# Kernel tuning notes

Measured on AMD Instinct MI355X. Metric: run time of the kernel, lower is better.

## Reference

```python
import jax, jax.numpy as jnp
import numpy as np

N_BLOCKS = 8
N_WIRES = 24
GAMMA, BETA, ALPHA = 0.1, 0.6, 0.15


def _apply_ry(state, w, theta):
    # RY(theta) = [[cos(t/2), -sin(t/2)], [sin(t/2), cos(t/2)]] on wire w.
    c = jnp.cos(theta * 0.5)
    s = jnp.sin(theta * 0.5)
    st = jnp.moveaxis(state, w, 0)  # (2, ...)
    new = jnp.stack([c * st[0] - s * st[1], s * st[0] + c * st[1]])
    return jnp.moveaxis(new, 0, w)


def _apply_cnot(state, ctrl, tgt):
    # Flip target bit where control bit == 1.
    st = jnp.moveaxis(state, (ctrl, tgt), (0, 1))  # (2, 2, ...)
    new = jnp.stack([st[0], st[1, ::-1]])
    return jnp.moveaxis(new, (0, 1), (ctrl, tgt))


def setup_inputs() -> dict:
    key = jax.random.key(0)
    angles = jax.random.normal(key, (N_BLOCKS, N_WIRES), dtype=jnp.float32)
    return {"angles": angles}


def reference(angles):
    n_blocks, n_wires = angles.shape  # static
    # Initial state |0...0>; RY and CNOT are real, so the state stays real.
    state = jnp.zeros((2,) * n_wires, dtype=angles.dtype).at[(0,) * n_wires].set(1.0)
    for k in range(n_blocks):
        for w in range(n_wires):
            state = _apply_ry(state, w, angles[k, w])
        for w in range(n_wires - 1):  # circular=False -> linear chain
            state = _apply_cnot(state, w, w + 1)
    probs = (state.reshape(-1) ** 2).reshape(2 ** n_wires, 1)  # |amp|^2
    easy_scale = 2.0 ** (n_wires - 1)
    x = (BETA * jnp.tanh(GAMMA * easy_scale * probs)) ** ALPHA
    return x - jnp.mean(x)
```

## Files before the change

### kernel.cpp

```cpp
#include <hip/hip_runtime.h>

#define NB 8
#define SSIZE (1u << 24)


__global__ void k_prep(const float* __restrict__ ang, double* __restrict__ dws) {
    int t = threadIdx.x;
    if (t == 0) dws[0] = 0.0;
    if (t < NB * 24) {
        double a = 0.5 * (double)ang[t];
        dws[8 + t]   = cos(a);
        dws[200 + t] = sin(a);
    }
}


__device__ __forceinline__ unsigned sw(unsigned f) {
    return f ^ (((f >> 3) ^ (f >> 5)) & 7u);
}

__device__ __forceinline__ void ry2d(double& a0, double& a1, double c, double s, bool ctl) {
    double w0 = c * a0 - s * a1;
    double w1 = s * a0 + c * a1;
    a0 = ctl ? w1 : w0;
    a1 = ctl ? w0 : w1;
}

template<int TB, int MODE>
__device__ __forceinline__ void stage8d(double4* x, double c, double s) {
#pragma unroll
    for (int j0 = 0; j0 < 8; ++j0) {
        if (j0 & (1 << TB)) continue;
        const int j1 = j0 | (1 << TB);
        const bool ctl = (MODE == 1) || (MODE == 0 && ((j0 >> (TB + 1)) & 1));
        ry2d(x[j0].x, x[j1].x, c, s, ctl);
        ry2d(x[j0].y, x[j1].y, c, s, ctl);
        ry2d(x[j0].z, x[j1].z, c, s, ctl);
        ry2d(x[j0].w, x[j1].w, c, s, ctl);
    }
}

template<int TB>
__device__ __forceinline__ void stage8d_rt(double4* x, double c, double s, bool ctl) {
#pragma unroll
    for (int j0 = 0; j0 < 8; ++j0) {
        if (j0 & (1 << TB)) continue;
        const int j1 = j0 | (1 << TB);
        ry2d(x[j0].x, x[j1].x, c, s, ctl);
        ry2d(x[j0].y, x[j1].y, c, s, ctl);
        ry2d(x[j0].z, x[j1].z, c, s, ctl);
        ry2d(x[j0].w, x[j1].w, c, s, ctl);
    }
}

__device__ __forceinline__ void coefs_d(unsigned lane, int lb, bool g,
                                        double c, double s, double& cA, double& cP) {
    bool b = (lane >> lb) & 1u;
    cA = g ? (b ? -s : s) : c;
    cP = g ? c : (b ? s : -s);
}


template<int CTRL>
__device__ __forceinline__ double dpp_xor_d(double v) {
    int lo = __builtin_amdgcn_mov_dpp(__double2loint(v), CTRL, 0xf, 0xf, true);
    int hi = __builtin_amdgcn_mov_dpp(__double2hiint(v), CTRL, 0xf, 0xf, true);
    return __hiloint2double(hi, lo);
}

template<int CTRL>
__device__ __forceinline__ void lane_stage_dpp(double4* x, double cA, double cP) {
#pragma unroll
    for (int j = 0; j < 8; ++j) {
        double px = dpp_xor_d<CTRL>(x[j].x);
        double py = dpp_xor_d<CTRL>(x[j].y);
        double pz = dpp_xor_d<CTRL>(x[j].z);
        double pw = dpp_xor_d<CTRL>(x[j].w);
        x[j].x = cA * x[j].x + cP * px;
        x[j].y = cA * x[j].y + cP * py;
        x[j].z = cA * x[j].z + cP * pz;
        x[j].w = cA * x[j].w + cP * pw;
    }
}

__device__ __forceinline__ void lane_stage_sw4(double4* x, double cA, double cP) {
#pragma unroll
    for (int j = 0; j < 8; ++j) {
        double px = __shfl_xor(x[j].x, 4, 64);
        double py = __shfl_xor(x[j].y, 4, 64);
        double pz = __shfl_xor(x[j].z, 4, 64);
        double pw = __shfl_xor(x[j].w, 4, 64);
        x[j].x = cA * x[j].x + cP * px;
        x[j].y = cA * x[j].y + cP * py;
        x[j].z = cA * x[j].z + cP * pz;
        x[j].w = cA * x[j].w + cP * pw;
    }
}

template<bool IS32>
__device__ __forceinline__ void swap_pair_d(double& a, double& b) {
    int alo = __double2loint(a), ahi = __double2hiint(a);
    int blo = __double2loint(b), bhi = __double2hiint(b);
    if (IS32) {
        auto r0 = __builtin_amdgcn_permlane32_swap(alo, blo, false, false);
        auto r1 = __builtin_amdgcn_permlane32_swap(ahi, bhi, false, false);
        alo = r0[0]; blo = r0[1]; ahi = r1[0]; bhi = r1[1];
    } else {
        auto r0 = __builtin_amdgcn_permlane16_swap(alo, blo, false, false);
        auto r1 = __builtin_amdgcn_permlane16_swap(ahi, bhi, false, false);
        alo = r0[0]; blo = r0[1]; ahi = r1[0]; bhi = r1[1];
    }
    a = __hiloint2double(ahi, alo);
    b = __hiloint2double(bhi, blo);
}

template<bool IS32>
__device__ __forceinline__ void stage_swap(double4* x, double c, double s, bool gsel) {
    double al = gsel ? s : c, be = gsel ? c : -s;
    double ga = gsel ? c : s, de = gsel ? -s : c;
#pragma unroll
    for (int p = 0; p < 4; ++p) {
        double4& A = x[2 * p];
        double4& B = x[2 * p + 1];
        swap_pair_d<IS32>(A.x, B.x); swap_pair_d<IS32>(A.y, B.y);
        swap_pair_d<IS32>(A.z, B.z); swap_pair_d<IS32>(A.w, B.w);
        double ux = A.x, vx = B.x, uy = A.y, vy = B.y;
        double uz = A.z, vz = B.z, uw = A.w, vw = B.w;
        A.x = al * ux + be * vx;  B.x = ga * ux + de * vx;
        A.y = al * uy + be * vy;  B.y = ga * uy + de * vy;
        A.z = al * uz + be * vz;  B.z = ga * uz + de * vz;
        A.w = al * uw + be * vw;  B.w = ga * uw + de * vw;
        swap_pair_d<IS32>(A.x, B.x); swap_pair_d<IS32>(A.y, B.y);
        swap_pair_d<IS32>(A.z, B.z); swap_pair_d<IS32>(A.w, B.w);
    }
}

__device__ __forceinline__ void dstages_d(double4* x, double c1, double s1, bool g1,
                                          double c0, double s0) {
#pragma unroll
    for (int j = 0; j < 8; ++j) {
        ry2d(x[j].x, x[j].z, c1, s1, g1);
        ry2d(x[j].y, x[j].w, c1, s1, g1);
        ry2d(x[j].x, x[j].y, c0, s0, false);
        ry2d(x[j].z, x[j].w, c0, s0, true);
    }
}

__device__ __forceinline__ float xform(float z) {
    float e2 = __builtin_amdgcn_exp2f(z * 2.8853900817779268f);
    float big = 1.0f - 2.0f * __builtin_amdgcn_rcpf(e2 + 1.0f);
    float z2 = z * z;
    float small_ = z * (1.0f - 0.33333333f * z2 * (1.0f - 0.4f * z2));
    float t = (z < 0.04f) ? small_ : big;
    return __builtin_amdgcn_exp2f(0.15f * __builtin_amdgcn_logf(0.6f * t));
}


__device__ __forceinline__ float4 lo4(const double4 v) {
    return make_float4(__int_as_float(__double2loint(v.x)),
                       __int_as_float(__double2loint(v.y)),
                       __int_as_float(__double2loint(v.z)),
                       __int_as_float(__double2loint(v.w)));
}
__device__ __forceinline__ float4 hi4(const double4 v) {
    return make_float4(__int_as_float(__double2hiint(v.x)),
                       __int_as_float(__double2hiint(v.y)),
                       __int_as_float(__double2hiint(v.z)),
                       __int_as_float(__double2hiint(v.w)));
}
__device__ __forceinline__ double4 mk4(const float4 h, const float4 l) {
    return make_double4(__hiloint2double(__float_as_int(h.x), __float_as_int(l.x)),
                        __hiloint2double(__float_as_int(h.y), __float_as_int(l.y)),
                        __hiloint2double(__float_as_int(h.z), __float_as_int(l.z)),
                        __hiloint2double(__float_as_int(h.w), __float_as_int(l.w)));
}

__device__ __forceinline__ void t_fwd_d(float4* T4, double4* x, unsigned tid,
                                        unsigned lane, unsigned hi, bool protect) {
    if (protect) __syncthreads();
#pragma unroll
    for (int jj = 0; jj < 8; ++jj) T4[sw(tid | (jj << 9))] = lo4(x[jj]);
    __syncthreads();
    float4 tl[8];
#pragma unroll
    for (int jj = 0; jj < 8; ++jj) tl[jj] = T4[sw(lane | (jj << 6) | hi)];
    __syncthreads();
#pragma unroll
    for (int jj = 0; jj < 8; ++jj) T4[sw(tid | (jj << 9))] = hi4(x[jj]);
    __syncthreads();
#pragma unroll
    for (int jj = 0; jj < 8; ++jj)
        x[jj] = mk4(T4[sw(lane | (jj << 6) | hi)], tl[jj]);
}

__device__ __forceinline__ void t_back_d(float4* T4, double4* x, unsigned tid,
                                         unsigned lane, unsigned hi) {
    __syncthreads();
#pragma unroll
    for (int jj = 0; jj < 8; ++jj) T4[sw(lane | (jj << 6) | hi)] = lo4(x[jj]);
    __syncthreads();
    float4 tl[8];
#pragma unroll
    for (int jj = 0; jj < 8; ++jj) tl[jj] = T4[sw(tid | (jj << 9))];
    __syncthreads();
#pragma unroll
    for (int jj = 0; jj < 8; ++jj) T4[sw(lane | (jj << 6) | hi)] = hi4(x[jj]);
    __syncthreads();
#pragma unroll
    for (int jj = 0; jj < 8; ++jj)
        x[jj] = mk4(T4[sw(tid | (jj << 9))], tl[jj]);
}

template<int START>
__device__ __forceinline__ void jj_trio_d(double4* x, const double* c, const double* s,
                                          bool top_on) {
    if (START == 0) {
        if (top_on) stage8d<2, 1>(x, c[0], s[0]);
        else        stage8d<2,-1>(x, c[0], s[0]);
    }
    if (START <= 1) stage8d<1, 0>(x, c[1], s[1]);
    stage8d<0, 0>(x, c[2], s[2]);
}

template<int N>
__device__ __forceinline__ void lane_ladder_v(double4* x, unsigned lane,
                                              const double* c, const double* s) {
    const bool hi5 = lane >= 32;
    stage_swap<true>(x, c[0], s[0], hi5);
    if (N > 1) stage_swap<false>(x, c[1], s[1], hi5);
    if (N > 2) { double cA, cP; coefs_d(lane, 3, (lane >> 4) & 1, c[2], s[2], cA, cP);
                 lane_stage_dpp<0x128>(x, cA, cP); }
    if (N > 3) { double cA, cP; coefs_d(lane, 2, (lane >> 3) & 1, c[3], s[3], cA, cP);
                 lane_stage_sw4(x, cA, cP); }
    if (N > 4) { double cA, cP; coefs_d(lane, 1, (lane >> 2) & 1, c[4], s[4], cA, cP);
                 lane_stage_dpp<0x4E>(x, cA, cP); }
    if (N > 5) { double cA, cP; coefs_d(lane, 0, (lane >> 1) & 1, c[5], s[5], cA, cP);
                 lane_stage_dpp<0xB1>(x, cA, cP); }
}

__device__ __forceinline__ double4 d4_of(const float4 f) {
    return make_double4((double)f.x, (double)f.y, (double)f.z, (double)f.w);
}
__device__ __forceinline__ float4 f4_of(const double4 d) {
    return make_float4((float)d.x, (float)d.y, (float)d.z, (float)d.w);
}

template<int I, int NBLK>
__device__ __forceinline__ void h_block(double4* x, float4* T4,
                                        const double* __restrict__ dws, int kbase,
                                        unsigned tid, unsigned lane, unsigned hi) {
    const double* C = dws + 8   + (kbase + I) * 24;
    const double* S = dws + 200 + (kbase + I) * 24;
    jj_trio_d<0>(x, C + 0, S + 0, false);
    t_fwd_d(T4, x, tid, lane, hi, I > 0);
    jj_trio_d<0>(x, C + 3, S + 3, (tid & 64u) != 0);
    lane_ladder_v<6 - I>(x, lane, C + 6, S + 6);
    if constexpr (I < NBLK - 1) {
        t_back_d(T4, x, tid, lane, hi);
        h_block<I + 1, NBLK>(x, T4, dws, kbase, tid, lane, hi);
    }
}

template<int NBLK, int INIT>
__global__ __launch_bounds__(512, 2) void k_H(float* __restrict__ st,
                                              const double* __restrict__ dws,
                                              int kbase) {
    __shared__ float4 T4[4096];
    const unsigned bid = blockIdx.x;
    const unsigned m = (bid >> 3) | ((bid & 7u) << 7);
    const unsigned tid = threadIdx.x;
    const unsigned lane = tid & 63u;
    const unsigned hi = (tid >> 6) << 9;
    const unsigned mbase4 = ((m & 3u) << 2) | ((m >> 2) << 4);
    float4* G4 = reinterpret_cast<float4*>(st);
    double4 x[8];

    if (INIT) {
        const double* C0 = dws + 8;
        const double* S0 = dws + 200;
        double P = 1.0;
#pragma unroll
        for (int b = 2; b <= 10; ++b) {
            unsigned g = ((m >> (b - 2)) ^ (m >> (b - 1))) & 1u;
            P *= g ? S0[23 - b] : C0[23 - b];
        }
        { unsigned g = ((m >> 9) ^ tid) & 1u; P *= g ? S0[12] : C0[12]; }
#pragma unroll
        for (int b = 12; b <= 19; ++b) {
            unsigned g = ((tid >> (b - 12)) ^ (tid >> (b - 11))) & 1u;
            P *= g ? S0[23 - b] : C0[23 - b];
        }
        double D[4];
#pragma unroll
        for (int d = 0; d < 4; ++d) {
            unsigned g0 = (d ^ (d >> 1)) & 1u;
            unsigned g1 = ((d >> 1) ^ m) & 1u;
            D[d] = (g0 ? S0[23] : C0[23]) * (g1 ? S0[22] : C0[22]);
        }
        unsigned t8 = (tid >> 8) & 1u;
#pragma unroll
        for (int jj = 0; jj < 8; ++jj) {
            unsigned g20 = (t8 ^ (unsigned)jj) & 1u;
            unsigned g21 = ((unsigned)jj ^ ((unsigned)jj >> 1)) & 1u;
            unsigned g22 = (((unsigned)jj >> 1) ^ ((unsigned)jj >> 2)) & 1u;
            unsigned g23 = (((unsigned)jj >> 2)) & 1u;
            double J = (g20 ? S0[3] : C0[3]) * (g21 ? S0[2] : C0[2]) *
                       (g22 ? S0[1] : C0[1]) * (g23 ? S0[0] : C0[0]);
            double PJ = P * J;
            x[jj] = make_double4(PJ * D[0], PJ * D[1], PJ * D[2], PJ * D[3]);
        }
    } else {
#pragma unroll
        for (int jj = 0; jj < 8; ++jj) {
            unsigned w = tid | (jj << 9);
            x[jj] = d4_of(G4[mbase4 | (w & 3u) | ((w >> 2) << 12)]);
        }
    }

    h_block<0, NBLK>(x, T4, dws, kbase, tid, lane, hi);

#pragma unroll
    for (int jj = 0; jj < 8; ++jj) {
        unsigned w = lane | (jj << 6) | hi;
        G4[mbase4 | (w & 3u) | ((w >> 2) << 12)] = f4_of(x[jj]);
    }
}

template<int NBLK, int FUSE>
__global__ __launch_bounds__(512, 2) void k_L(float* __restrict__ st,
                                              double* __restrict__ dws,
                                              int kbase) {
    __shared__ float4 T4[4096];
    const unsigned m = blockIdx.x;
    const unsigned tid = threadIdx.x;
    const unsigned lane = tid & 63u;
    const unsigned hi = (tid >> 6) << 9;
    float4* G4 = reinterpret_cast<float4*>(st) + (m << 12);
    double4 x[8];
#pragma unroll
    for (int jj = 0; jj < 8; ++jj) x[jj] = d4_of(G4[tid + (jj << 9)]);

#pragma unroll
    for (int i = 0; i < NBLK; ++i) {
        const double* C = dws + 8   + (kbase + i) * 24;
        const double* S = dws + 200 + (kbase + i) * 24;
        if (i >= 2) {
            double cA, cP; coefs_d(lane, 1, (m & 1u) != 0, C[10], S[10], cA, cP);
            lane_stage_dpp<0x4E>(x, cA, cP);
        }
        if (i >= 1) {
            double cA, cP; coefs_d(lane, 0, (lane >> 1) & 1, C[11], S[11], cA, cP);
            lane_stage_dpp<0xB1>(x, cA, cP);
        }
        stage8d_rt<2>(x, C[12], S[12], (lane & 1u) != 0);
        stage8d<1, 0>(x, C[13], S[13]);
        stage8d<0, 0>(x, C[14], S[14]);
        t_fwd_d(T4, x, tid, lane, hi, i > 0);
        if (tid & 64u) stage8d<2, 1>(x, C[15], S[15]);
        else           stage8d<2,-1>(x, C[15], S[15]);
        stage8d<1, 0>(x, C[16], S[16]);
        stage8d<0, 0>(x, C[17], S[17]);
        stage_swap<true >(x, C[18], S[18], lane >= 32);
        stage_swap<false>(x, C[19], S[19], lane >= 32);
        { double cA, cP; coefs_d(lane, 3, (lane >> 4) & 1, C[20], S[20], cA, cP);
          lane_stage_dpp<0x128>(x, cA, cP); }
        { double cA, cP; coefs_d(lane, 2, (lane >> 3) & 1, C[21], S[21], cA, cP);
          lane_stage_sw4(x, cA, cP); }
        dstages_d(x, C[22], S[22], ((lane >> 2) & 1u) != 0,
                  C[23], S[23]);
        if (i < NBLK - 1) t_back_d(T4, x, tid, lane, hi);
    }

    if (FUSE) {
        double lsum = 0.0;
        __syncthreads();
#pragma unroll
        for (int jj = 0; jj < 8; ++jj) {
            double* v = &x[jj].x;
            float4 o;
            float* ov = &o.x;
#pragma unroll
            for (int d = 0; d < 4; ++d) {
                float z = (float)(838860.8 * v[d] * v[d]);
                float xf = xform(z);
                ov[d] = xf;
                lsum += (double)xf;
            }
            unsigned t4 = ((lane >> 2) & 0xFu) | ((unsigned)jj << 4)
                        | (((tid >> 6) & 7u) << 7) | ((lane & 3u) << 10);
            T4[sw(t4)] = o;
        }
        __syncthreads();
#pragma unroll
        for (int jj = 0; jj < 8; ++jj)
            G4[tid | (jj << 9)] = T4[sw(tid | (jj << 9))];
#pragma unroll
        for (int o = 32; o > 0; o >>= 1) lsum += __shfl_down(lsum, o, 64);
        __syncthreads();
        double* wsum = reinterpret_cast<double*>(T4);
        if ((tid & 63u) == 0) wsum[tid >> 6] = lsum;
        __syncthreads();
        if (tid == 0) {
            double b = 0.0;
#pragma unroll
            for (int i = 0; i < 8; ++i) b += wsum[i];
            atomicAdd(dws, b);
        }
    } else {
#pragma unroll
        for (int jj = 0; jj < 8; ++jj)
            G4[lane | (jj << 6) | hi] = f4_of(x[jj]);
    }
}

__global__ void k_final(float* __restrict__ st, const double* __restrict__ dws) {
    unsigned idx = blockIdx.x * blockDim.x + threadIdx.x;
    unsigned stride = gridDim.x * blockDim.x;
    float mean = (float)(dws[0] * (1.0 / 16777216.0));
    float4* G4 = reinterpret_cast<float4*>(st);
    for (unsigned q = idx; q < (SSIZE / 4); q += stride) {
        float4 v = G4[q];
        v.x -= mean; v.y -= mean; v.z -= mean; v.w -= mean;
        G4[q] = v;
    }
}

extern "C" void kernel_launch(void* const* d_in, const int* in_sizes, int n_in,
                              void* d_out, int out_size, void* d_ws, size_t ws_size,
                              hipStream_t stream) {
    const float* ang = (const float*)d_in[0];
    float* st = (float*)d_out;
    double* dws = (double*)d_ws;

    k_prep<<<1, 256, 0, stream>>>(ang, dws);
    k_H<3, 1><<<1024, 512, 0, stream>>>(st, dws, 1);
    k_L<3, 0><<<1024, 512, 0, stream>>>(st, dws, 1);
    k_H<3, 0><<<1024, 512, 0, stream>>>(st, dws, 4);
    k_L<3, 0><<<1024, 512, 0, stream>>>(st, dws, 4);
    k_H<1, 0><<<1024, 512, 0, stream>>>(st, dws, 7);
    k_L<1, 1><<<1024, 512, 0, stream>>>(st, dws, 7);
    k_final<<<4096, 256, 0, stream>>>(st, dws);
}
```

Baseline: 561.4 us.

## Halve LDS transpose buffer to allow more blocks per CU

The shared-memory transpose moves from a 64 KB float4 buffer, exchanged as lo/hi 32-bit halves, to a 32 KB double buffer exchanged one double component at a time over four rounds. The fused output epilogue is split into two half-writes so it fits the smaller buffer. Launch bounds rise from 2 to 6 blocks per CU to exploit the lower LDS footprint. The cost is more barriers per transpose (8 instead of 4-5) and 8-byte LDS accesses, and the higher occupancy target may cap registers and cause spills of the double4[8] state.

```diff
diff --git a/kernel.cpp b/kernel.cpp
--- a/kernel.cpp
+++ b/kernel.cpp
@@ -156,59 +156,34 @@
 }
 
 
-__device__ __forceinline__ float4 lo4(const double4 v) {
-    return make_float4(__int_as_float(__double2loint(v.x)),
-                       __int_as_float(__double2loint(v.y)),
-                       __int_as_float(__double2loint(v.z)),
-                       __int_as_float(__double2loint(v.w)));
-}
-__device__ __forceinline__ float4 hi4(const double4 v) {
-    return make_float4(__int_as_float(__double2hiint(v.x)),
-                       __int_as_float(__double2hiint(v.y)),
-                       __int_as_float(__double2hiint(v.z)),
-                       __int_as_float(__double2hiint(v.w)));
-}
-__device__ __forceinline__ double4 mk4(const float4 h, const float4 l) {
-    return make_double4(__hiloint2double(__float_as_int(h.x), __float_as_int(l.x)),
-                        __hiloint2double(__float_as_int(h.y), __float_as_int(l.y)),
-                        __hiloint2double(__float_as_int(h.z), __float_as_int(l.z)),
-                        __hiloint2double(__float_as_int(h.w), __float_as_int(l.w)));
-}
-
-__device__ __forceinline__ void t_fwd_d(float4* T4, double4* x, unsigned tid,
-                                        unsigned lane, unsigned hi, bool protect) {
-    if (protect) __syncthreads();
-#pragma unroll
-    for (int jj = 0; jj < 8; ++jj) T4[sw(tid | (jj << 9))] = lo4(x[jj]);
-    __syncthreads();
-    float4 tl[8];
-#pragma unroll
-    for (int jj = 0; jj < 8; ++jj) tl[jj] = T4[sw(lane | (jj << 6) | hi)];
-    __syncthreads();
-#pragma unroll
-    for (int jj = 0; jj < 8; ++jj) T4[sw(tid | (jj << 9))] = hi4(x[jj]);
-    __syncthreads();
-#pragma unroll
-    for (int jj = 0; jj < 8; ++jj)
-        x[jj] = mk4(T4[sw(lane | (jj << 6) | hi)], tl[jj]);
-}
-
-__device__ __forceinline__ void t_back_d(float4* T4, double4* x, unsigned tid,
+__device__ __forceinline__ void t_fwd_dd(double* T2, double4* x, unsigned tid,
                                          unsigned lane, unsigned hi) {
-    __syncthreads();
-#pragma unroll
-    for (int jj = 0; jj < 8; ++jj) T4[sw(lane | (jj << 6) | hi)] = lo4(x[jj]);
-    __syncthreads();
-    float4 tl[8];
-#pragma unroll
-    for (int jj = 0; jj < 8; ++jj) tl[jj] = T4[sw(tid | (jj << 9))];
-    __syncthreads();
-#pragma unroll
-    for (int jj = 0; jj < 8; ++jj) T4[sw(lane | (jj << 6) | hi)] = hi4(x[jj]);
-    __syncthreads();
-#pragma unroll
-    for (int jj = 0; jj < 8; ++jj)
-        x[jj] = mk4(T4[sw(tid | (jj << 9))], tl[jj]);
+#pragma unroll
+    for (int c = 0; c < 4; ++c) {
+#pragma unroll
+        for (int jj = 0; jj < 8; ++jj)
+            T2[sw(tid | (jj << 9))] = (&x[jj].x)[c];
+        __syncthreads();
+#pragma unroll
+        for (int jj = 0; jj < 8; ++jj)
+            (&x[jj].x)[c] = T2[sw(lane | (jj << 6) | hi)];
+        __syncthreads();
+    }
+}
+
+__device__ __forceinline__ void t_back_dd(double* T2, double4* x, unsigned tid,
+                                          unsigned lane, unsigned hi) {
+#pragma unroll
+    for (int c = 0; c < 4; ++c) {
+#pragma unroll
+        for (int jj = 0; jj < 8; ++jj)
+            T2[sw(lane | (jj << 6) | hi)] = (&x[jj].x)[c];
+        __syncthreads();
+#pragma unroll
+        for (int jj = 0; jj < 8; ++jj)
+            (&x[jj].x)[c] = T2[sw(tid | (jj << 9))];
+        __syncthreads();
+    }
 }
 
 template<int START>
@@ -246,26 +221,26 @@
 }
 
 template<int I, int NBLK>
-__device__ __forceinline__ void h_block(double4* x, float4* T4,
+__device__ __forceinline__ void h_block(double4* x, double* T2,
                                         const double* __restrict__ dws, int kbase,
                                         unsigned tid, unsigned lane, unsigned hi) {
     const double* C = dws + 8   + (kbase + I) * 24;
     const double* S = dws + 200 + (kbase + I) * 24;
     jj_trio_d<0>(x, C + 0, S + 0, false);
-    t_fwd_d(T4, x, tid, lane, hi, I > 0);
+    t_fwd_dd(T2, x, tid, lane, hi);
     jj_trio_d<0>(x, C + 3, S + 3, (tid & 64u) != 0);
     lane_ladder_v<6 - I>(x, lane, C + 6, S + 6);
     if constexpr (I < NBLK - 1) {
-        t_back_d(T4, x, tid, lane, hi);
-        h_block<I + 1, NBLK>(x, T4, dws, kbase, tid, lane, hi);
+        t_back_dd(T2, x, tid, lane, hi);
+        h_block<I + 1, NBLK>(x, T2, dws, kbase, tid, lane, hi);
     }
 }
 
 template<int NBLK, int INIT>
-__global__ __launch_bounds__(512, 2) void k_H(float* __restrict__ st,
+__global__ __launch_bounds__(512, 6) void k_H(float* __restrict__ st,
                                               const double* __restrict__ dws,
                                               int kbase) {
-    __shared__ float4 T4[4096];
+    __shared__ __align__(16) double T2[4096];
     const unsigned bid = blockIdx.x;
     const unsigned m = (bid >> 3) | ((bid & 7u) << 7);
     const unsigned tid = threadIdx.x;
@@ -317,7 +292,7 @@
         }
     }
 
-    h_block<0, NBLK>(x, T4, dws, kbase, tid, lane, hi);
+    h_block<0, NBLK>(x, T2, dws, kbase, tid, lane, hi);
 
 #pragma unroll
     for (int jj = 0; jj < 8; ++jj) {
@@ -327,10 +302,10 @@
 }
 
 template<int NBLK, int FUSE>
-__global__ __launch_bounds__(512, 2) void k_L(float* __restrict__ st,
+__global__ __launch_bounds__(512, 6) void k_L(float* __restrict__ st,
                                               double* __restrict__ dws,
                                               int kbase) {
-    __shared__ float4 T4[4096];
+    __shared__ __align__(16) double T2[4096];
     const unsigned m = blockIdx.x;
     const unsigned tid = threadIdx.x;
     const unsigned lane = tid & 63u;
@@ -355,7 +330,7 @@
         stage8d_rt<2>(x, C[12], S[12], (lane & 1u) != 0);
         stage8d<1, 0>(x, C[13], S[13]);
         stage8d<0, 0>(x, C[14], S[14]);
-        t_fwd_d(T4, x, tid, lane, hi, i > 0);
+        t_fwd_dd(T2, x, tid, lane, hi);
         if (tid & 64u) stage8d<2, 1>(x, C[15], S[15]);
         else           stage8d<2,-1>(x, C[15], S[15]);
         stage8d<1, 0>(x, C[16], S[16]);
@@ -368,17 +343,16 @@
           lane_stage_sw4(x, cA, cP); }
         dstages_d(x, C[22], S[22], ((lane >> 2) & 1u) != 0,
                   C[23], S[23]);
-        if (i < NBLK - 1) t_back_d(T4, x, tid, lane, hi);
+        if (i < NBLK - 1) t_back_dd(T2, x, tid, lane, hi);
     }
 
     if (FUSE) {
+        float4 o[8];
         double lsum = 0.0;
-        __syncthreads();
 #pragma unroll
         for (int jj = 0; jj < 8; ++jj) {
             double* v = &x[jj].x;
-            float4 o;
-            float* ov = &o.x;
+            float* ov = &o[jj].x;
 #pragma unroll
             for (int d = 0; d < 4; ++d) {
                 float z = (float)(838860.8 * v[d] * v[d]);
@@ -386,24 +360,36 @@
                 ov[d] = xf;
                 lsum += (double)xf;
             }
-            unsigned t4 = ((lane >> 2) & 0xFu) | ((unsigned)jj << 4)
-                        | (((tid >> 6) & 7u) << 7) | ((lane & 3u) << 10);
-            T4[sw(t4)] = o;
-        }
-        __syncthreads();
-#pragma unroll
-        for (int jj = 0; jj < 8; ++jj)
-            G4[tid | (jj << 9)] = T4[sw(tid | (jj << 9))];
-#pragma unroll
-        for (int o = 32; o > 0; o >>= 1) lsum += __shfl_down(lsum, o, 64);
-        __syncthreads();
-        double* wsum = reinterpret_cast<double*>(T4);
-        if ((tid & 63u) == 0) wsum[tid >> 6] = lsum;
+        }
+        float4* TF = reinterpret_cast<float4*>(T2);
+        const unsigned t4b = ((lane >> 2) & 0xFu) | (((tid >> 6) & 7u) << 7)
+                           | ((lane & 3u) << 10);
+        if (!(lane & 2u)) {
+#pragma unroll
+            for (int jj = 0; jj < 8; ++jj) TF[sw(t4b | (jj << 4))] = o[jj];
+        }
+        __syncthreads();
+#pragma unroll
+        for (int jj = 0; jj < 4; ++jj)
+            G4[tid | (jj << 9)] = TF[sw(tid | (jj << 9))];
+        __syncthreads();
+        if (lane & 2u) {
+#pragma unroll
+            for (int jj = 0; jj < 8; ++jj) TF[sw((t4b ^ 2048u) | (jj << 4))] = o[jj];
+        }
+        __syncthreads();
+#pragma unroll
+        for (int jj = 4; jj < 8; ++jj)
+            G4[tid | (jj << 9)] = TF[sw(tid | ((jj - 4) << 9))];
+#pragma unroll
+        for (int os = 32; os > 0; os >>= 1) lsum += __shfl_down(lsum, os, 64);
+        __syncthreads();
+        if ((tid & 63u) == 0) T2[tid >> 6] = lsum;
         __syncthreads();
         if (tid == 0) {
             double b = 0.0;
 #pragma unroll
-            for (int i = 0; i < 8; ++i) b += wsum[i];
+            for (int i = 0; i < 8; ++i) b += T2[i];
             atomicAdd(dws, b);
         }
     } else {
```

Result: slower. 755.5 us (+34.6%).
